# Kernel tuning notes

Hardware: AMD Instinct MI355X
Metric: run time of the kernel (lower is better)

The kernel has to match this reference:

```python
import jax, jax.numpy as jnp
import numpy as np

N_NODES = 100000
N_EDGES = 1600000
HIDDEN = 128
SLOPE = 0.2


def setup_inputs() -> dict:
    key = jax.random.key(0)
    k1, k2, k3, k4, k5, k6 = jax.random.split(key, 6)
    x = jax.random.normal(k1, (N_NODES, HIDDEN), dtype=jnp.float32)
    W_l = jax.random.normal(k2, (HIDDEN, HIDDEN), dtype=jnp.float32) * (1.0 / np.sqrt(HIDDEN))
    W_r = jax.random.normal(k3, (HIDDEN, HIDDEN), dtype=jnp.float32) * (1.0 / np.sqrt(HIDDEN))
    alpha = jax.random.uniform(k4, (N_EDGES, 1), dtype=jnp.float32)
    src = jax.random.randint(k5, (N_EDGES,), 0, N_NODES, dtype=jnp.int32)
    dst = jax.random.randint(k6, (N_EDGES,), 0, N_NODES, dtype=jnp.int32)
    return {"x": x, "W_l": W_l, "W_r": W_r, "alpha": alpha, "src": src, "dst": dst}


def reference(x, W_l, W_r, alpha, src, dst):
    # x: [N, D]; W_l, W_r: [D, D] (nn.Linear weight layout, y = x @ W.T)
    # src, dst: [E] edge endpoints; alpha: [E, 1] scalar edge weights.
    n_nodes = x.shape[0]
    hl_all = x @ W_l.T                     # [N, D]
    hr_all = x @ W_r.T                     # [N, D]
    h_l = hl_all[src]                      # [E, D] gather by source
    h_r = hr_all[dst]                      # [E, D] gather by destination
    z = jax.nn.leaky_relu((h_l + h_r) * alpha, negative_slope=SLOPE)  # [E, D]
    e = jnp.sum(z, axis=1, keepdims=True)  # [E, 1] per-edge score
    # Destination-grouped (edge) softmax, numerically stable.
    e_max = jax.ops.segment_max(e, dst, num_segments=n_nodes)          # [N, 1]
    ex = jnp.exp(e - e_max[dst])                                       # [E, 1]
    denom = jax.ops.segment_sum(ex, dst, num_segments=n_nodes)        # [N, 1]
    a = ex / denom[dst]                                                # [E, 1]
    # Weighted scatter-sum of source features to destinations.
    msg = x[src] * a                                                   # [E, D]
    return jax.ops.segment_sum(msg, dst, num_segments=n_nodes)        # [N, D]
```

## Files before the change

kernel.cpp:

```cpp
#include <hip/hip_runtime.h>
#include <hip/hip_fp16.h>

#define HID 128
#define BCAP 16384
#define GCAP 10240

struct h8 { __half2 a, b, c, d; };

typedef _Float16 half8v __attribute__((ext_vector_type(8)));
typedef _Float16 h2v    __attribute__((ext_vector_type(2)));
typedef float floatx4  __attribute__((ext_vector_type(4)));

static __device__ __forceinline__ float fdot2h(__half2 a, __half2 b, float c) {
    h2v av, bv;
    __builtin_memcpy(&av, &a, 4);
    __builtin_memcpy(&bv, &b, 4);
    return __builtin_amdgcn_fdot2(av, bv, c, false);
}

static __device__ __forceinline__ __half2 hmax2p(__half2 a, __half2 b) {
    h2v av, bv, rv;
    __builtin_memcpy(&av, &a, 4);
    __builtin_memcpy(&bv, &b, 4);
    rv = __builtin_elementwise_max(av, bv);
    __half2 r;
    __builtin_memcpy(&r, &rv, 4);
    return r;
}

__global__ __launch_bounds__(512) void prep_kernel(
    const float* __restrict__ x, h8* __restrict__ xh,
    const float* __restrict__ Wl, const float* __restrict__ Wr,
    __half* __restrict__ Wh,
    const int* __restrict__ dst, const int* __restrict__ src,
    const float* __restrict__ alpha, int* __restrict__ bcount,
    int2* __restrict__ bs, int nbe, int nbx, int ntot, int e)
{
    __shared__ int cnt[256], lsc[256], lbase[256], scn[256];
    __shared__ int2 sa_s[4096];
    __shared__ unsigned char bin_s[4096];

    int bid = blockIdx.x;
    int t   = threadIdx.x;

    if (bid >= nbe + nbx) {
        int i = (bid - nbe - nbx) * 4096 + t * 8;
        const float* W = (i < 16384) ? Wl : Wr;
        int ii = i & 16383;
        const float4* p = (const float4*)(W + ii);
        float4 v0 = p[0], v1 = p[1];
        h8 o;
        o.a = __float22half2_rn(make_float2(v0.x, v0.y));
        o.b = __float22half2_rn(make_float2(v0.z, v0.w));
        o.c = __float22half2_rn(make_float2(v1.x, v1.y));
        o.d = __float22half2_rn(make_float2(v1.z, v1.w));
        *(h8*)(Wh + i) = o;
        return;
    }
    if (bid >= nbe) {
        int i = (bid - nbe) * 512 + t;
        if (i < ntot) {
            const float4* p = (const float4*)x + (size_t)i * 2;
            float4 v0 = p[0], v1 = p[1];
            h8 o;
            o.a = __float22half2_rn(make_float2(v0.x, v0.y));
            o.b = __float22half2_rn(make_float2(v0.z, v0.w));
            o.c = __float22half2_rn(make_float2(v1.x, v1.y));
            o.d = __float22half2_rn(make_float2(v1.z, v1.w));
            xh[i] = o;
        }
        return;
    }

    int base = bid * 4096;
    if (t < 256) cnt[t] = 0;
    __syncthreads();

    int d[8], bn[8], lp[8];
    bool val[8];
    #pragma unroll
    for (int j = 0; j < 8; ++j) {
        int i = base + t + j * 512;
        val[j] = i < e;
        d[j]   = val[j] ? dst[i] : 0;
        bn[j]  = d[j] >> 9;
        lp[j]  = val[j] ? atomicAdd(&cnt[bn[j]], 1) : 0;
    }
    __syncthreads();

    int v = (t < 256) ? cnt[t] : 0;
    if (t < 256) scn[t] = v;
    #pragma unroll
    for (int off = 1; off < 256; off <<= 1) {
        int add = (t < 256 && t >= off) ? scn[t - off] : 0;
        __syncthreads();
        if (t < 256) scn[t] += add;
        __syncthreads();
    }
    if (t < 256) {
        lsc[t]   = scn[t] - v;
        lbase[t] = v ? atomicAdd(&bcount[t], v) : 0;
    }
    __syncthreads();

    #pragma unroll
    for (int j = 0; j < 8; ++j) {
        int i = base + t + j * 512;
        if (val[j]) {
            int pos = lsc[bn[j]] + lp[j];
            sa_s[pos]  = make_int2(src[i] | ((d[j] & 511) << 17),
                                   __float_as_int(alpha[i]));
            bin_s[pos] = (unsigned char)bn[j];
        }
    }
    __syncthreads();

    int tot = min(4096, e - base);
    for (int i = t; i < tot; i += 512) {
        int bb  = bin_s[i];
        int pos = lbase[bb] + (i - lsc[bb]);
        if (pos < BCAP) bs[(size_t)bb * BCAP + pos] = sa_s[i];
    }
}

__global__ __launch_bounds__(256) void scan2_kernel(
    const int* __restrict__ bcount, int* __restrict__ bpref,
    int* __restrict__ offs, int nbins, int n, int e)
{
    __shared__ int s[256];
    int t = threadIdx.x;
    int v = (t < nbins) ? min(bcount[t], BCAP) : 0;
    s[t] = v;
    __syncthreads();
    #pragma unroll
    for (int off = 1; off < 256; off <<= 1) {
        int add = (t >= off) ? s[t - off] : 0;
        __syncthreads();
        s[t] += add;
        __syncthreads();
    }
    if (t < nbins) bpref[t] = s[t] - v;
    if (t == 0) offs[n] = e;
}

__global__ __launch_bounds__(256) void gemm_kernel(
    const __half* __restrict__ xh, const __half* __restrict__ Wh,
    __half* __restrict__ Hl, __half* __restrict__ Hr, int n)
{
    int t    = threadIdx.x;
    int w    = blockIdx.x * 4 + (t >> 6);
    int mat  = (w >= 6250) ? 1 : 0;
    int rt   = w - mat * 6250;
    int row0 = rt * 16;

    int lane = t & 63;
    int fr   = lane & 15;
    int kg   = (lane >> 4) * 8;

    const __half* xrow  = xh + (size_t)(row0 + fr) * HID + kg;
    const __half* wbase = Wh + (size_t)mat * 16384 + (size_t)fr * HID + kg;

    floatx4 acc[8];
    #pragma unroll
    for (int nt = 0; nt < 8; ++nt) acc[nt] = (floatx4){0.f, 0.f, 0.f, 0.f};

    #pragma unroll
    for (int kt = 0; kt < 4; ++kt) {
        half8v a = *(const half8v*)(xrow + kt * 32);
        #pragma unroll
        for (int nt = 0; nt < 8; ++nt) {
            half8v b = *(const half8v*)(wbase + (size_t)nt * 16 * HID + kt * 32);
            acc[nt] = __builtin_amdgcn_mfma_f32_16x16x32_f16(a, b, acc[nt], 0, 0, 0);
        }
    }

    __half* H = mat ? Hr : Hl;
    int orow0 = row0 + (lane >> 4) * 4;
    #pragma unroll
    for (int r = 0; r < 4; ++r) {
        size_t rb = (size_t)(orow0 + r) * HID + fr;
        #pragma unroll
        for (int nt = 0; nt < 8; ++nt)
            H[rb + nt * 16] = __float2half(acc[nt][r]);
    }
}

__global__ __launch_bounds__(512) void group_kernel(
    const int2* __restrict__ bs, const int* __restrict__ bcount,
    const int* __restrict__ bpref, int* __restrict__ offs,
    int2* __restrict__ edges, int n)
{
    __shared__ int2 sal[GCAP];
    __shared__ int s[512], p[512];

    int b = blockIdx.x, t = threadIdx.x;
    int cnt  = min(bcount[b], BCAP);
    int base = bpref[b];
    const int2* mybs = bs + (size_t)b * BCAP;

    s[t] = 0;
    __syncthreads();
    for (int i = t; i < cnt; i += 512)
        atomicAdd(&s[((unsigned)mybs[i].x) >> 17], 1);
    __syncthreads();
    int v = s[t];
    #pragma unroll
    for (int off = 1; off < 512; off <<= 1) {
        int add = (t >= off) ? s[t - off] : 0;
        __syncthreads();
        s[t] += add;
        __syncthreads();
    }
    int excl = s[t] - v;
    p[t] = excl;
    int node = b * 512 + t;
    if (node < n) offs[node] = base + excl;
    __syncthreads();

    if (cnt <= GCAP) {
        for (int i = t; i < cnt; i += 512) {
            int2 r = mybs[i];
            int dl = ((unsigned)r.x) >> 17;
            r.x &= 0x1FFFF;
            int pp = atomicAdd(&p[dl], 1);
            sal[pp] = r;
        }
        __syncthreads();
        for (int i = t; i < cnt; i += 512)
            edges[base + i] = sal[i];
    } else {
        for (int i = t; i < cnt; i += 512) {
            int2 r = mybs[i];
            int dl = ((unsigned)r.x) >> 17;
            r.x &= 0x1FFFF;
            int pp = atomicAdd(&p[dl], 1);
            edges[base + pp] = r;
        }
    }
}

__global__ __launch_bounds__(256) void score_kernel(
    const h8* __restrict__ hl, const h8* __restrict__ hr,
    int2* __restrict__ edges, const int* __restrict__ offs,
    float2* __restrict__ maxdenom, int n)
{
    int node = blockIdx.x * 4 + (threadIdx.x >> 6);
    if (node >= n) return;
    int lane = threadIdx.x & 63;
    int sub  = lane >> 4;
    int sl   = lane & 15;

    int beg = offs[node];
    int end = offs[node + 1];
    if (beg == end) return;

    h8 hv = hr[(size_t)node * 16 + sl];
    const __half2 c02  = __float2half2_rn(0.2f);
    const __half2 one2 = __float2half2_rn(1.0f);

    int2 r0A, r1A, r0B, r1B;
    bool v0A, v1A, v0B, v1B;
    {
        int e0 = beg + sub, e1 = beg + 4 + sub;
        v0A = e0 < end; v1A = e1 < end;
        r0A = v0A ? edges[e0] : make_int2(0, 0);
        r1A = v1A ? edges[e1] : make_int2(0, 0);
    }

    float m = -3.0e38f, den = 0.f;
    for (int base = beg; base < end; base += 8) {
        {
            int e0 = base + 8 + sub, e1 = base + 12 + sub;
            v0B = e0 < end; v1B = e1 < end;
            r0B = v0B ? edges[e0] : make_int2(0, 0);
            r1B = v1B ? edges[e1] : make_int2(0, 0);
        }
        h8 row0 = hl[(size_t)r0A.x * 16 + sl];
        h8 row1 = hl[(size_t)r1A.x * 16 + sl];

        float S0 = 0.f, S1 = 0.f;
        __half2 z;
        z = __hadd2(row0.a, hv.a); z = hmax2p(z, __hmul2(z, c02)); S0 = fdot2h(z, one2, S0);
        z = __hadd2(row0.b, hv.b); z = hmax2p(z, __hmul2(z, c02)); S0 = fdot2h(z, one2, S0);
        z = __hadd2(row0.c, hv.c); z = hmax2p(z, __hmul2(z, c02)); S0 = fdot2h(z, one2, S0);
        z = __hadd2(row0.d, hv.d); z = hmax2p(z, __hmul2(z, c02)); S0 = fdot2h(z, one2, S0);
        z = __hadd2(row1.a, hv.a); z = hmax2p(z, __hmul2(z, c02)); S1 = fdot2h(z, one2, S1);
        z = __hadd2(row1.b, hv.b); z = hmax2p(z, __hmul2(z, c02)); S1 = fdot2h(z, one2, S1);
        z = __hadd2(row1.c, hv.c); z = hmax2p(z, __hmul2(z, c02)); S1 = fdot2h(z, one2, S1);
        z = __hadd2(row1.d, hv.d); z = hmax2p(z, __hmul2(z, c02)); S1 = fdot2h(z, one2, S1);

        S0 += __shfl_xor(S0, 1); S1 += __shfl_xor(S1, 1);
        S0 += __shfl_xor(S0, 2); S1 += __shfl_xor(S1, 2);
        S0 += __shfl_xor(S0, 4); S1 += __shfl_xor(S1, 4);
        S0 += __shfl_xor(S0, 8); S1 += __shfl_xor(S1, 8);

        float p0 = __int_as_float(r0A.y) * S0;
        float p1 = __int_as_float(r1A.y) * S1;
        if (!v0A) p0 = -3.0e38f;
        if (!v1A) p1 = -3.0e38f;
        if (sl == 0) {
            if (v0A) edges[base + sub].y     = __float_as_int(p0);
            if (v1A) edges[base + 4 + sub].y = __float_as_int(p1);
        }

        float pm = fmaxf(p0, p1);
        pm = fmaxf(pm, __shfl_xor(pm, 16));
        pm = fmaxf(pm, __shfl_xor(pm, 32));
        float mn = fmaxf(m, pm);
        float sc = __expf(m - mn);
        float w0 = __expf(p0 - mn);
        float w1 = __expf(p1 - mn);
        den = den * sc + w0 + w1;
        m = mn;

        r0A = r0B; r1A = r1B; v0A = v0B; v1A = v1B;
    }

    den += __shfl_xor(den, 16);
    den += __shfl_xor(den, 32);
    if (lane == 0) maxdenom[node] = make_float2(m, 1.f / den);
}

__global__ __launch_bounds__(256) void agg_kernel(
    const h8* __restrict__ xh, const int2* __restrict__ edges,
    const int* __restrict__ offs, const float2* __restrict__ maxdenom,
    float* __restrict__ out, int n)
{
    int node = blockIdx.x * 4 + (threadIdx.x >> 6);
    if (node >= n) return;
    int lane = threadIdx.x & 63;
    int sub  = lane >> 4;
    int sl   = lane & 15;

    float* orow = out + (size_t)node * HID + (sl << 3);
    int beg = offs[node];
    int end = offs[node + 1];
    if (beg == end) {
        if (sub == 0) {
            *(float4*)orow       = make_float4(0.f, 0.f, 0.f, 0.f);
            *(float4*)(orow + 4) = make_float4(0.f, 0.f, 0.f, 0.f);
        }
        return;
    }

    float2 md = maxdenom[node];
    const float m = md.x, inv = md.y;

    int2 r0A, r1A, r0B, r1B;
    bool v0A, v1A, v0B, v1B;
    {
        int e0 = beg + sub, e1 = beg + 4 + sub;
        v0A = e0 < end; v1A = e1 < end;
        r0A = v0A ? edges[e0] : make_int2(0, 0);
        r1A = v1A ? edges[e1] : make_int2(0, 0);
    }

    float4 aca = make_float4(0.f, 0.f, 0.f, 0.f);
    float4 acb = make_float4(0.f, 0.f, 0.f, 0.f);

    for (int base = beg; base < end; base += 8) {
        {
            int e0 = base + 8 + sub, e1 = base + 12 + sub;
            v0B = e0 < end; v1B = e1 < end;
            r0B = v0B ? edges[e0] : make_int2(0, 0);
            r1B = v1B ? edges[e1] : make_int2(0, 0);
        }
        h8 row0 = xh[(size_t)r0A.x * 16 + sl];
        h8 row1 = xh[(size_t)r1A.x * 16 + sl];

        float w0 = v0A ? __expf(__int_as_float(r0A.y) - m) * inv : 0.f;
        float w1 = v1A ? __expf(__int_as_float(r1A.y) - m) * inv : 0.f;
        __half2 w2 = __floats2half2_rn(w0, w1);

        __half2 plo, phi;
        plo = __halves2half2(__low2half(row0.a),  __low2half(row1.a));
        phi = __halves2half2(__high2half(row0.a), __high2half(row1.a));
        aca.x = fdot2h(plo, w2, aca.x);
        aca.y = fdot2h(phi, w2, aca.y);
        plo = __halves2half2(__low2half(row0.b),  __low2half(row1.b));
        phi = __halves2half2(__high2half(row0.b), __high2half(row1.b));
        aca.z = fdot2h(plo, w2, aca.z);
        aca.w = fdot2h(phi, w2, aca.w);
        plo = __halves2half2(__low2half(row0.c),  __low2half(row1.c));
        phi = __halves2half2(__high2half(row0.c), __high2half(row1.c));
        acb.x = fdot2h(plo, w2, acb.x);
        acb.y = fdot2h(phi, w2, acb.y);
        plo = __halves2half2(__low2half(row0.d),  __low2half(row1.d));
        phi = __halves2half2(__high2half(row0.d), __high2half(row1.d));
        acb.z = fdot2h(plo, w2, acb.z);
        acb.w = fdot2h(phi, w2, acb.w);

        r0A = r0B; r1A = r1B; v0A = v0B; v1A = v1B;
    }

    aca.x += __shfl_xor(aca.x, 16); aca.x += __shfl_xor(aca.x, 32);
    aca.y += __shfl_xor(aca.y, 16); aca.y += __shfl_xor(aca.y, 32);
    aca.z += __shfl_xor(aca.z, 16); aca.z += __shfl_xor(aca.z, 32);
    aca.w += __shfl_xor(aca.w, 16); aca.w += __shfl_xor(aca.w, 32);
    acb.x += __shfl_xor(acb.x, 16); acb.x += __shfl_xor(acb.x, 32);
    acb.y += __shfl_xor(acb.y, 16); acb.y += __shfl_xor(acb.y, 32);
    acb.z += __shfl_xor(acb.z, 16); acb.z += __shfl_xor(acb.z, 32);
    acb.w += __shfl_xor(acb.w, 16); acb.w += __shfl_xor(acb.w, 32);

    if (sub == 0) {
        *(float4*)orow       = aca;
        *(float4*)(orow + 4) = acb;
    }
}

extern "C" void kernel_launch(void* const* d_in, const int* in_sizes, int n_in,
                              void* d_out, int out_size, void* d_ws, size_t ws_size,
                              hipStream_t stream)
{
    const float* x     = (const float*)d_in[0];
    const float* Wl    = (const float*)d_in[1];
    const float* Wr    = (const float*)d_in[2];
    const float* alpha = (const float*)d_in[3];
    const int*   src   = (const int*)d_in[4];
    const int*   dst   = (const int*)d_in[5];
    const int n = in_sizes[0] / HID;
    const int e = in_sizes[4];
    float* out = (float*)d_out;

    const int nbins = (n + 511) / 512;

    char* ws = (char*)d_ws;
    size_t off = 0;
    auto carve = [&](size_t bytes) -> void* {
        void* p = ws + off;
        off = (off + bytes + 255) & ~(size_t)255;
        return p;
    };
    __half* hl_h    = (__half*)carve((size_t)n * HID * sizeof(__half));
    __half* hr_h    = (__half*)carve((size_t)n * HID * sizeof(__half));
    __half* xh      = (__half*)carve((size_t)n * HID * sizeof(__half));
    __half* Wh      = (__half*)carve((size_t)2 * HID * HID * sizeof(__half));
    int*    offs    = (int*)carve((size_t)(n + 1) * sizeof(int));
    int*    bcount  = (int*)carve(256 * sizeof(int));
    int*    bpref   = (int*)carve(256 * sizeof(int));
    int2*   edges   = (int2*)carve((size_t)e * sizeof(int2));
    int2*   bs      = (int2*)carve((size_t)nbins * BCAP * sizeof(int2));
    float2* maxden  = (float2*)carve((size_t)n * sizeof(float2));

    (void)hipMemsetAsync(bcount, 0, 256 * sizeof(int), stream);

    int nbe = (e + 4095) / 4096;
    int nbx = (n * 16 + 511) / 512;
    prep_kernel<<<nbe + nbx + 8, 512, 0, stream>>>(
        x, (h8*)xh, Wl, Wr, Wh, dst, src, alpha, bcount, bs,
        nbe, nbx, n * 16, e);

    gemm_kernel<<<3125, 256, 0, stream>>>(xh, Wh, hl_h, hr_h, n);

    scan2_kernel<<<1, 256, 0, stream>>>(bcount, bpref, offs, nbins, n, e);
    group_kernel<<<nbins, 512, 0, stream>>>(bs, bcount, bpref, offs, edges, n);

    score_kernel<<<(n + 3) / 4, 256, 0, stream>>>(
        (const h8*)hl_h, (const h8*)hr_h, edges, offs, maxden, n);
    agg_kernel<<<(n + 3) / 4, 256, 0, stream>>>((const h8*)xh, edges, offs, maxden, out, n);
}
```

Baseline: 232.5 us.

## Fuse score and aggregation into one online-softmax kernel with interleaved hl/x rows

Merges the score and aggregation kernels into a single per-destination pass that uses an online softmax: the running max rescales the denominator and the weighted feature accumulator, and normalisation happens once at the end. Each node's projected h_l row and half-precision x row are stored together in one 512-byte block, so both gathers for a source node hit adjacent memory. This removes the second pass over edges, the write-back of per-edge scores and the max/denominator array. The cost is extra rescale work whenever the max grows and a larger interleaved buffer that the GEMM writes with a strided layout.

```diff
diff --git a/kernel.cpp b/kernel.cpp
--- a/kernel.cpp
+++ b/kernel.cpp
@@ -29,7 +29,7 @@
 }
 
 __global__ __launch_bounds__(512) void prep_kernel(
-    const float* __restrict__ x, h8* __restrict__ xh,
+    const float* __restrict__ x, h8* __restrict__ hlx,
     const float* __restrict__ Wl, const float* __restrict__ Wr,
     __half* __restrict__ Wh,
     const int* __restrict__ dst, const int* __restrict__ src,
@@ -67,7 +67,7 @@
             o.b = __float22half2_rn(make_float2(v0.z, v0.w));
             o.c = __float22half2_rn(make_float2(v1.x, v1.y));
             o.d = __float22half2_rn(make_float2(v1.z, v1.w));
-            xh[i] = o;
+            hlx[((size_t)(i >> 4)) * 32 + 16 + (i & 15)] = o;
         }
         return;
     }
@@ -144,8 +144,8 @@
 }
 
 __global__ __launch_bounds__(256) void gemm_kernel(
-    const __half* __restrict__ xh, const __half* __restrict__ Wh,
-    __half* __restrict__ Hl, __half* __restrict__ Hr, int n)
+    __half* __restrict__ hlx_h, const __half* __restrict__ Wh,
+    __half* __restrict__ hr_h, int n)
 {
     int t    = threadIdx.x;
     int w    = blockIdx.x * 4 + (t >> 6);
@@ -157,7 +157,7 @@
     int fr   = lane & 15;
     int kg   = (lane >> 4) * 8;
 
-    const __half* xrow  = xh + (size_t)(row0 + fr) * HID + kg;
+    const __half* xrow  = hlx_h + (size_t)(row0 + fr) * 256 + 128 + kg;
     const __half* wbase = Wh + (size_t)mat * 16384 + (size_t)fr * HID + kg;
 
     floatx4 acc[8];
@@ -174,11 +174,12 @@
         }
     }
 
-    __half* H = mat ? Hr : Hl;
+    __half* H      = mat ? hr_h : hlx_h;
+    int     stride = mat ? 128 : 256;
     int orow0 = row0 + (lane >> 4) * 4;
     #pragma unroll
     for (int r = 0; r < 4; ++r) {
-        size_t rb = (size_t)(orow0 + r) * HID + fr;
+        size_t rb = (size_t)(orow0 + r) * stride + fr;
         #pragma unroll
         for (int nt = 0; nt < 8; ++nt)
             H[rb + nt * 16] = __float2half(acc[nt][r]);
@@ -239,10 +240,10 @@
     }
 }
 
-__global__ __launch_bounds__(256) void score_kernel(
-    const h8* __restrict__ hl, const h8* __restrict__ hr,
-    int2* __restrict__ edges, const int* __restrict__ offs,
-    float2* __restrict__ maxdenom, int n)
+__global__ __launch_bounds__(256) void edge_kernel(
+    const h8* __restrict__ hlx, const h8* __restrict__ hr,
+    const int2* __restrict__ edges, const int* __restrict__ offs,
+    float* __restrict__ out, int n, int etot)
 {
     int node = blockIdx.x * 4 + (threadIdx.x >> 6);
     if (node >= n) return;
@@ -250,13 +251,23 @@
     int sub  = lane >> 4;
     int sl   = lane & 15;
 
+    float* orow = out + (size_t)node * HID + (sl << 3);
     int beg = offs[node];
     int end = offs[node + 1];
-    if (beg == end) return;
+    end = min(end, etot);
+    if (end < beg) end = beg;
+    if (beg == end) {
+        if (sub == 0) {
+            *(float4*)orow       = make_float4(0.f, 0.f, 0.f, 0.f);
+            *(float4*)(orow + 4) = make_float4(0.f, 0.f, 0.f, 0.f);
+        }
+        return;
+    }
 
     h8 hv = hr[(size_t)node * 16 + sl];
-    const __half2 c02  = __float2half2_rn(0.2f);
+    const __half2 c02 = __float2half2_rn(0.2f);
     const __half2 one2 = __float2half2_rn(1.0f);
+    const int smax = n - 1;
 
     int2 r0A, r1A, r0B, r1B;
     bool v0A, v1A, v0B, v1B;
@@ -268,6 +279,9 @@
     }
 
     float m = -3.0e38f, den = 0.f;
+    float4 aca = make_float4(0.f, 0.f, 0.f, 0.f);
+    float4 acb = make_float4(0.f, 0.f, 0.f, 0.f);
+
     for (int base = beg; base < end; base += 8) {
         {
             int e0 = base + 8 + sub, e1 = base + 12 + sub;
@@ -275,19 +289,25 @@
             r0B = v0B ? edges[e0] : make_int2(0, 0);
             r1B = v1B ? edges[e1] : make_int2(0, 0);
         }
-        h8 row0 = hl[(size_t)r0A.x * 16 + sl];
-        h8 row1 = hl[(size_t)r1A.x * 16 + sl];
+        int s0 = min(r0A.x, smax);
+        int s1 = min(r1A.x, smax);
+        const h8* blk0 = hlx + (size_t)s0 * 32;
+        const h8* blk1 = hlx + (size_t)s1 * 32;
+        h8 hl0 = blk0[sl];
+        h8 x0  = blk0[16 + sl];
+        h8 hl1 = blk1[sl];
+        h8 x1  = blk1[16 + sl];
 
         float S0 = 0.f, S1 = 0.f;
         __half2 z;
-        z = __hadd2(row0.a, hv.a); z = hmax2p(z, __hmul2(z, c02)); S0 = fdot2h(z, one2, S0);
-        z = __hadd2(row0.b, hv.b); z = hmax2p(z, __hmul2(z, c02)); S0 = fdot2h(z, one2, S0);
-        z = __hadd2(row0.c, hv.c); z = hmax2p(z, __hmul2(z, c02)); S0 = fdot2h(z, one2, S0);
-        z = __hadd2(row0.d, hv.d); z = hmax2p(z, __hmul2(z, c02)); S0 = fdot2h(z, one2, S0);
-        z = __hadd2(row1.a, hv.a); z = hmax2p(z, __hmul2(z, c02)); S1 = fdot2h(z, one2, S1);
-        z = __hadd2(row1.b, hv.b); z = hmax2p(z, __hmul2(z, c02)); S1 = fdot2h(z, one2, S1);
-        z = __hadd2(row1.c, hv.c); z = hmax2p(z, __hmul2(z, c02)); S1 = fdot2h(z, one2, S1);
-        z = __hadd2(row1.d, hv.d); z = hmax2p(z, __hmul2(z, c02)); S1 = fdot2h(z, one2, S1);
+        z = __hadd2(hl0.a, hv.a); z = hmax2p(z, __hmul2(z, c02)); S0 = fdot2h(z, one2, S0);
+        z = __hadd2(hl0.b, hv.b); z = hmax2p(z, __hmul2(z, c02)); S0 = fdot2h(z, one2, S0);
+        z = __hadd2(hl0.c, hv.c); z = hmax2p(z, __hmul2(z, c02)); S0 = fdot2h(z, one2, S0);
+        z = __hadd2(hl0.d, hv.d); z = hmax2p(z, __hmul2(z, c02)); S0 = fdot2h(z, one2, S0);
+        z = __hadd2(hl1.a, hv.a); z = hmax2p(z, __hmul2(z, c02)); S1 = fdot2h(z, one2, S1);
+        z = __hadd2(hl1.b, hv.b); z = hmax2p(z, __hmul2(z, c02)); S1 = fdot2h(z, one2, S1);
+        z = __hadd2(hl1.c, hv.c); z = hmax2p(z, __hmul2(z, c02)); S1 = fdot2h(z, one2, S1);
+        z = __hadd2(hl1.d, hv.d); z = hmax2p(z, __hmul2(z, c02)); S1 = fdot2h(z, one2, S1);
 
         S0 += __shfl_xor(S0, 1); S1 += __shfl_xor(S1, 1);
         S0 += __shfl_xor(S0, 2); S1 += __shfl_xor(S1, 2);
@@ -298,101 +318,45 @@
         float p1 = __int_as_float(r1A.y) * S1;
         if (!v0A) p0 = -3.0e38f;
         if (!v1A) p1 = -3.0e38f;
-        if (sl == 0) {
-            if (v0A) edges[base + sub].y     = __float_as_int(p0);
-            if (v1A) edges[base + 4 + sub].y = __float_as_int(p1);
-        }
 
         float pm = fmaxf(p0, p1);
         pm = fmaxf(pm, __shfl_xor(pm, 16));
         pm = fmaxf(pm, __shfl_xor(pm, 32));
-        float mn = fmaxf(m, pm);
-        float sc = __expf(m - mn);
-        float w0 = __expf(p0 - mn);
-        float w1 = __expf(p1 - mn);
-        den = den * sc + w0 + w1;
-        m = mn;
+        if (pm > m) {
+            float sc = __expf(m - pm);
+            den *= sc;
+            aca.x *= sc; aca.y *= sc; aca.z *= sc; aca.w *= sc;
+            acb.x *= sc; acb.y *= sc; acb.z *= sc; acb.w *= sc;
+            m = pm;
+        }
+        float w0 = __expf(p0 - m);
+        float w1 = __expf(p1 - m);
+        den += w0 + w1;
+
+        __half2 w2 = __floats2half2_rn(w0, w1);
+        __half2 plo, phi;
+        plo = __halves2half2(__low2half(x0.a),  __low2half(x1.a));
+        phi = __halves2half2(__high2half(x0.a), __high2half(x1.a));
+        aca.x = fdot2h(plo, w2, aca.x);
+        aca.y = fdot2h(phi, w2, aca.y);
+        plo = __halves2half2(__low2half(x0.b),  __low2half(x1.b));
+        phi = __halves2half2(__high2half(x0.b), __high2half(x1.b));
+        aca.z = fdot2h(plo, w2, aca.z);
+        aca.w = fdot2h(phi, w2, aca.w);
+        plo = __halves2half2(__low2half(x0.c),  __low2half(x1.c));
+        phi = __halves2half2(__high2half(x0.c), __high2half(x1.c));
+        acb.x = fdot2h(plo, w2, acb.x);
+        acb.y = fdot2h(phi, w2, acb.y);
+        plo = __halves2half2(__low2half(x0.d),  __low2half(x1.d));
+        phi = __halves2half2(__high2half(x0.d), __high2half(x1.d));
+        acb.z = fdot2h(plo, w2, acb.z);
+        acb.w = fdot2h(phi, w2, acb.w);
 
         r0A = r0B; r1A = r1B; v0A = v0B; v1A = v1B;
     }
 
     den += __shfl_xor(den, 16);
     den += __shfl_xor(den, 32);
-    if (lane == 0) maxdenom[node] = make_float2(m, 1.f / den);
-}
-
-__global__ __launch_bounds__(256) void agg_kernel(
-    const h8* __restrict__ xh, const int2* __restrict__ edges,
-    const int* __restrict__ offs, const float2* __restrict__ maxdenom,
-    float* __restrict__ out, int n)
-{
-    int node = blockIdx.x * 4 + (threadIdx.x >> 6);
-    if (node >= n) return;
-    int lane = threadIdx.x & 63;
-    int sub  = lane >> 4;
-    int sl   = lane & 15;
-
-    float* orow = out + (size_t)node * HID + (sl << 3);
-    int beg = offs[node];
-    int end = offs[node + 1];
-    if (beg == end) {
-        if (sub == 0) {
-            *(float4*)orow       = make_float4(0.f, 0.f, 0.f, 0.f);
-            *(float4*)(orow + 4) = make_float4(0.f, 0.f, 0.f, 0.f);
-        }
-        return;
-    }
-
-    float2 md = maxdenom[node];
-    const float m = md.x, inv = md.y;
-
-    int2 r0A, r1A, r0B, r1B;
-    bool v0A, v1A, v0B, v1B;
-    {
-        int e0 = beg + sub, e1 = beg + 4 + sub;
-        v0A = e0 < end; v1A = e1 < end;
-        r0A = v0A ? edges[e0] : make_int2(0, 0);
-        r1A = v1A ? edges[e1] : make_int2(0, 0);
-    }
-
-    float4 aca = make_float4(0.f, 0.f, 0.f, 0.f);
-    float4 acb = make_float4(0.f, 0.f, 0.f, 0.f);
-
-    for (int base = beg; base < end; base += 8) {
-        {
-            int e0 = base + 8 + sub, e1 = base + 12 + sub;
-            v0B = e0 < end; v1B = e1 < end;
-            r0B = v0B ? edges[e0] : make_int2(0, 0);
-            r1B = v1B ? edges[e1] : make_int2(0, 0);
-        }
-        h8 row0 = xh[(size_t)r0A.x * 16 + sl];
-        h8 row1 = xh[(size_t)r1A.x * 16 + sl];
-
-        float w0 = v0A ? __expf(__int_as_float(r0A.y) - m) * inv : 0.f;
-        float w1 = v1A ? __expf(__int_as_float(r1A.y) - m) * inv : 0.f;
-        __half2 w2 = __floats2half2_rn(w0, w1);
-
-        __half2 plo, phi;
-        plo = __halves2half2(__low2half(row0.a),  __low2half(row1.a));
-        phi = __halves2half2(__high2half(row0.a), __high2half(row1.a));
-        aca.x = fdot2h(plo, w2, aca.x);
-        aca.y = fdot2h(phi, w2, aca.y);
-        plo = __halves2half2(__low2half(row0.b),  __low2half(row1.b));
-        phi = __halves2half2(__high2half(row0.b), __high2half(row1.b));
-        aca.z = fdot2h(plo, w2, aca.z);
-        aca.w = fdot2h(phi, w2, aca.w);
-        plo = __halves2half2(__low2half(row0.c),  __low2half(row1.c));
-        phi = __halves2half2(__high2half(row0.c), __high2half(row1.c));
-        acb.x = fdot2h(plo, w2, acb.x);
-        acb.y = fdot2h(phi, w2, acb.y);
-        plo = __halves2half2(__low2half(row0.d),  __low2half(row1.d));
-        phi = __halves2half2(__high2half(row0.d), __high2half(row1.d));
-        acb.z = fdot2h(plo, w2, acb.z);
-        acb.w = fdot2h(phi, w2, acb.w);
-
-        r0A = r0B; r1A = r1B; v0A = v0B; v1A = v1B;
-    }
-
     aca.x += __shfl_xor(aca.x, 16); aca.x += __shfl_xor(aca.x, 32);
     aca.y += __shfl_xor(aca.y, 16); aca.y += __shfl_xor(aca.y, 32);
     aca.z += __shfl_xor(aca.z, 16); aca.z += __shfl_xor(aca.z, 32);
@@ -403,8 +367,11 @@
     acb.w += __shfl_xor(acb.w, 16); acb.w += __shfl_xor(acb.w, 32);
 
     if (sub == 0) {
-        *(float4*)orow       = aca;
-        *(float4*)(orow + 4) = acb;
+        float inv = 1.f / den;
+        *(float4*)orow =
+            make_float4(aca.x * inv, aca.y * inv, aca.z * inv, aca.w * inv);
+        *(float4*)(orow + 4) =
+            make_float4(acb.x * inv, acb.y * inv, acb.z * inv, acb.w * inv);
     }
 }
 
@@ -431,31 +398,28 @@
         off = (off + bytes + 255) & ~(size_t)255;
         return p;
     };
-    __half* hl_h    = (__half*)carve((size_t)n * HID * sizeof(__half));
+    __half* hlx_h   = (__half*)carve((size_t)n * 256 * sizeof(__half));
     __half* hr_h    = (__half*)carve((size_t)n * HID * sizeof(__half));
-    __half* xh      = (__half*)carve((size_t)n * HID * sizeof(__half));
     __half* Wh      = (__half*)carve((size_t)2 * HID * HID * sizeof(__half));
     int*    offs    = (int*)carve((size_t)(n + 1) * sizeof(int));
     int*    bcount  = (int*)carve(256 * sizeof(int));
     int*    bpref   = (int*)carve(256 * sizeof(int));
     int2*   edges   = (int2*)carve((size_t)e * sizeof(int2));
     int2*   bs      = (int2*)carve((size_t)nbins * BCAP * sizeof(int2));
-    float2* maxden  = (float2*)carve((size_t)n * sizeof(float2));
 
     (void)hipMemsetAsync(bcount, 0, 256 * sizeof(int), stream);
 
     int nbe = (e + 4095) / 4096;
     int nbx = (n * 16 + 511) / 512;
     prep_kernel<<<nbe + nbx + 8, 512, 0, stream>>>(
-        x, (h8*)xh, Wl, Wr, Wh, dst, src, alpha, bcount, bs,
+        x, (h8*)hlx_h, Wl, Wr, Wh, dst, src, alpha, bcount, bs,
         nbe, nbx, n * 16, e);
 
-    gemm_kernel<<<3125, 256, 0, stream>>>(xh, Wh, hl_h, hr_h, n);
+    gemm_kernel<<<3125, 256, 0, stream>>>(hlx_h, Wh, hr_h, n);
 
     scan2_kernel<<<1, 256, 0, stream>>>(bcount, bpref, offs, nbins, n, e);
     group_kernel<<<nbins, 512, 0, stream>>>(bs, bcount, bpref, offs, edges, n);
 
-    score_kernel<<<(n + 3) / 4, 256, 0, stream>>>(
-        (const h8*)hl_h, (const h8*)hr_h, edges, offs, maxden, n);
-    agg_kernel<<<(n + 3) / 4, 256, 0, stream>>>((const h8*)xh, edges, offs, maxden, out, n);
-}
+    edge_kernel<<<(n + 3) / 4, 256, 0, stream>>>(
+        (const h8*)hlx_h, (const h8*)hr_h, edges, offs, out, n, e);
+}
```

Measured after the change: 220.2 us. 1.06x faster.
